# Performance work log

Hardware: AMD Instinct MI355X
Metric: run time of the kernel (lower is better)

The kernel has to match this reference:

```python
import jax, jax.numpy as jnp
import numpy as np

N_NODES = 100000
N_EDGES = 1600000
EMB = 128
EDGE_DIMS = [6, 3]
BN_EPS = 1e-5


def setup_inputs() -> dict:
    key = jax.random.key(0)
    ks = jax.random.split(key, 16)
    inp = {
        "node_feats": jax.random.normal(ks[0], (N_NODES, EMB), jnp.float32),
        "edge_feat_0": jax.random.uniform(ks[1], (N_EDGES, EDGE_DIMS[0]), jnp.float32),
        "edge_feat_1": jax.random.uniform(ks[2], (N_EDGES, EDGE_DIMS[1]), jnp.float32),
        "src": jax.random.randint(ks[3], (N_EDGES,), 0, N_NODES, jnp.int32),
        "dst": jax.random.randint(ks[4], (N_EDGES,), 0, N_NODES, jnp.int32),
    }
    # edge embedding linears (MLP num_layers==1 -> plain Linear)
    s0 = 1.0 / np.sqrt(EDGE_DIMS[0])
    s1 = 1.0 / np.sqrt(EDGE_DIMS[1])
    inp["We0"] = jax.random.uniform(ks[5], (EDGE_DIMS[0], EMB), jnp.float32, -s0, s0)
    inp["be0"] = jax.random.uniform(ks[6], (EMB,), jnp.float32, -s0, s0)
    inp["We1"] = jax.random.uniform(ks[7], (EDGE_DIMS[1], EMB), jnp.float32, -s1, s1)
    inp["be1"] = jax.random.uniform(ks[8], (EMB,), jnp.float32, -s1, s1)
    # mlp: Linear(emb, 2*emb) -> ReLU -> Linear(2*emb, emb)
    sm = 1.0 / np.sqrt(EMB)
    sh = 1.0 / np.sqrt(2 * EMB)
    inp["W1"] = jax.random.uniform(ks[9], (EMB, 2 * EMB), jnp.float32, -sm, sm)
    inp["b1"] = jax.random.uniform(ks[10], (2 * EMB,), jnp.float32, -sm, sm)
    inp["W2"] = jax.random.uniform(ks[11], (2 * EMB, EMB), jnp.float32, -sh, sh)
    inp["b2"] = jax.random.uniform(ks[12], (EMB,), jnp.float32, -sh, sh)
    # batch norm affine params
    inp["gamma"] = jnp.ones((EMB,), jnp.float32)
    inp["beta"] = jnp.zeros((EMB,), jnp.float32)
    return inp


def reference(node_feats, edge_feat_0, edge_feat_1, src, dst,
              We0, be0, We1, be1, W1, b1, W2, b2, gamma, beta):
    n_nodes = node_feats.shape[0]
    # per-family edge embeddings, summed
    edge_embs = (edge_feat_0 @ We0 + be0) + (edge_feat_1 @ We1 + be1)  # [E, D]
    # u_add_e: gather src node feats, add edge emb
    msgs = node_feats[src] + edge_embs  # [E, D]
    # scatter-sum to destination nodes
    agg = jax.ops.segment_sum(msgs, dst, num_segments=n_nodes)  # [N, D]
    # MLP: Linear -> ReLU -> Linear
    h = jax.nn.relu(agg @ W1 + b1) @ W2 + b2  # [N, D]
    # BatchNorm1d (training mode: batch statistics, biased variance)
    mean = jnp.mean(h, axis=0)
    var = jnp.var(h, axis=0)
    h = (h - mean) * jax.lax.rsqrt(var + BN_EPS) * gamma + beta
    return h
```

## Files before the change

kernel.cpp:

```cpp
#include <hip/hip_runtime.h>

#define N_NODES 100000
#define N_EDGES 1600000
#define EMB 128
#define BM 16
#define NSLAB 64
#define BN_EPS 1e-5f

#define SCAN_BLK 512
#define NB_SCAN ((N_NODES + SCAN_BLK - 1) / SCAN_BLK)
#define NPAD (NB_SCAN * SCAN_BLK)

typedef short short8 __attribute__((ext_vector_type(8)));
typedef float floatx4 __attribute__((ext_vector_type(4)));

__device__ __forceinline__ ushort f2bf(float x) {
    unsigned u = __float_as_uint(x);
    u += 0x7fffu + ((u >> 16) & 1u);
    return (ushort)(u >> 16);
}
__device__ __forceinline__ float bf2f(ushort u) {
    return __uint_as_float(((unsigned)u) << 16);
}
__device__ __forceinline__ float lo2f(unsigned p) {
    return __uint_as_float(p << 16);
}
__device__ __forceinline__ float hi2f(unsigned p) {
    return __uint_as_float(p & 0xffff0000u);
}

__global__ __launch_bounds__(256) void setup_kernel(
    const float* __restrict__ nf, ushort* __restrict__ nfbf,
    const int* __restrict__ dst, int* __restrict__ counts,
    const float* __restrict__ W1, const float* __restrict__ W2,
    ushort* __restrict__ w1f, ushort* __restrict__ w2f)
{
    int gtid = blockIdx.x * 256 + threadIdx.x;
    long gstride = (long)gridDim.x * 256;

    if (gtid < 65536) {
        int idx = gtid;
        int i = idx & 7;
        int lane = (idx >> 3) & 63;
        int kloc = ((lane >> 4) << 3) + i;
        int nloc = lane & 15;
        if (idx < 32768) {
            int ks = (idx >> 9) & 3, nt = idx >> 11;
            w1f[idx] = f2bf(W1[(ks * 32 + kloc) * 256 + nt * 16 + nloc]);
        } else {
            int j = idx - 32768;
            int ks = (j >> 9) & 7, nt = j >> 12;
            w2f[j] = f2bf(W2[(ks * 32 + kloc) * 128 + nt * 16 + nloc]);
        }
    }

    long total = (long)N_NODES * EMB / 4;
    for (long p = gtid; p < total; p += gstride) {
        float4 v = ((const float4*)nf)[p];
        ushort4 o;
        o.x = f2bf(v.x); o.y = f2bf(v.y); o.z = f2bf(v.z); o.w = f2bf(v.w);
        ((ushort4*)nfbf)[p] = o;
    }

    for (long e = gtid; e < N_EDGES; e += gstride)
        atomicAdd(&counts[dst[e]], 1);
}

__global__ __launch_bounds__(SCAN_BLK) void scan_blocksum_kernel(
    const int* __restrict__ counts, int* __restrict__ blockSums)
{
    __shared__ int red[SCAN_BLK];
    int t = threadIdx.x;
    int i = blockIdx.x * SCAN_BLK + t;
    red[t] = (i < N_NODES) ? counts[i] : 0;
    __syncthreads();
    for (int s = SCAN_BLK / 2; s > 0; s >>= 1) {
        if (t < s) red[t] += red[t + s];
        __syncthreads();
    }
    if (t == 0) blockSums[blockIdx.x] = red[0];
}

__global__ __launch_bounds__(256) void scan_blockoffsets_kernel(int* __restrict__ blockSums)
{
    __shared__ int s[256];
    int t = threadIdx.x;
    int orig = (t < NB_SCAN) ? blockSums[t] : 0;
    s[t] = orig;
    __syncthreads();
    for (int off = 1; off < 256; off <<= 1) {
        int v = (t >= off) ? s[t - off] : 0;
        __syncthreads();
        s[t] += v;
        __syncthreads();
    }
    if (t < NB_SCAN) blockSums[t] = s[t] - orig;
}

__global__ __launch_bounds__(SCAN_BLK) void scan_final_kernel(
    const int* __restrict__ counts, const int* __restrict__ blockSums,
    int* __restrict__ offsets, int* __restrict__ cursor)
{
    __shared__ int s[SCAN_BLK];
    int t = threadIdx.x;
    int i = blockIdx.x * SCAN_BLK + t;
    int orig = (i < N_NODES) ? counts[i] : 0;
    s[t] = orig;
    __syncthreads();
    for (int off = 1; off < SCAN_BLK; off <<= 1) {
        int v = (t >= off) ? s[t - off] : 0;
        __syncthreads();
        s[t] += v;
        __syncthreads();
    }
    int excl = s[t] - orig + blockSums[blockIdx.x];
    if (i < N_NODES) { offsets[i] = excl; cursor[i] = excl; }
    if (i == N_NODES) offsets[N_NODES] = N_EDGES;
}

__global__ __launch_bounds__(256) void scatter24_kernel(
    const int* __restrict__ src, const int* __restrict__ dst,
    const float* __restrict__ ef0, const float* __restrict__ ef1,
    int* __restrict__ cursor, int* __restrict__ rec24)
{
    int e = blockIdx.x * 256 + threadIdx.x;
    if (e >= N_EDGES) return;
    int t = dst[e];
    int pos = atomicAdd(&cursor[t], 1);

    const float2* p0 = (const float2*)(ef0 + (long)e * 6);
    float2 q0 = p0[0], q1 = p0[1], q2 = p0[2];
    const float* p1 = ef1 + (long)e * 3;
    float g0 = p1[0], g1 = p1[1], g2 = p1[2];

    unsigned u0 = (unsigned)f2bf(q0.x) | ((unsigned)f2bf(q0.y) << 16);
    unsigned u1 = (unsigned)f2bf(q1.x) | ((unsigned)f2bf(q1.y) << 16);
    unsigned u2 = (unsigned)f2bf(q2.x) | ((unsigned)f2bf(q2.y) << 16);
    unsigned u3 = (unsigned)f2bf(g0)   | ((unsigned)f2bf(g1) << 16);
    unsigned u4 = (unsigned)f2bf(g2);

    int2* out = (int2*)(rec24 + (long)pos * 6);
    out[0] = make_int2(src[e], (int)u0);
    out[1] = make_int2((int)u1, (int)u2);
    out[2] = make_int2((int)u3, (int)u4);
}

__global__ __launch_bounds__(256, 8) void gather4_kernel(
    const ushort* __restrict__ nfbf, const int* __restrict__ rec24,
    const int* __restrict__ offsets,
    const float* __restrict__ We0, const float* __restrict__ be0,
    const float* __restrict__ We1, const float* __restrict__ be1,
    float* __restrict__ agg)
{
    int wv = threadIdx.x >> 6, lane = threadIdx.x & 63;
    int n = blockIdx.x * 4 + wv;
    if (n >= N_NODES) return;
    int q = lane >> 4, lp = lane & 15;

    int beg = offsets[n], end = offsets[n + 1];
    float4 accA = make_float4(0.f, 0.f, 0.f, 0.f);
    float4 accB = make_float4(0.f, 0.f, 0.f, 0.f);
    float fs0 = 0.f, fs1 = 0.f, fs2 = 0.f, fs3 = 0.f, fs4 = 0.f,
          fs5 = 0.f, fs6 = 0.f, fs7 = 0.f, fs8 = 0.f;
    const int4* nf16 = (const int4*)nfbf;

    int base = beg;
    for (; base + 64 <= end; base += 64) {
        const int2* rp = (const int2*)(rec24 + (long)(base + lane) * 6);
        int2 ra = rp[0], rb = rp[1], rc = rp[2];
        int sid = ra.x;
        fs0 += lo2f((unsigned)ra.y); fs1 += hi2f((unsigned)ra.y);
        fs2 += lo2f((unsigned)rb.x); fs3 += hi2f((unsigned)rb.x);
        fs4 += lo2f((unsigned)rb.y); fs5 += hi2f((unsigned)rb.y);
        fs6 += lo2f((unsigned)rc.x); fs7 += hi2f((unsigned)rc.x);
        fs8 += lo2f((unsigned)rc.y);
#pragma unroll 4
        for (int j = 0; j < 16; ++j) {
            int s = __shfl(sid, 4 * j + q);
            int4 nv = nf16[(long)s * 16 + lp];
            accA.x += lo2f((unsigned)nv.x); accA.y += hi2f((unsigned)nv.x);
            accA.z += lo2f((unsigned)nv.y); accA.w += hi2f((unsigned)nv.y);
            accB.x += lo2f((unsigned)nv.z); accB.y += hi2f((unsigned)nv.z);
            accB.z += lo2f((unsigned)nv.w); accB.w += hi2f((unsigned)nv.w);
        }
    }
    if (base < end) {
        int m = end - base;
        int sid = 0;
        if (lane < m) {
            const int2* rp = (const int2*)(rec24 + (long)(base + lane) * 6);
            int2 ra = rp[0], rb = rp[1], rc = rp[2];
            sid = ra.x;
            fs0 += lo2f((unsigned)ra.y); fs1 += hi2f((unsigned)ra.y);
            fs2 += lo2f((unsigned)rb.x); fs3 += hi2f((unsigned)rb.x);
            fs4 += lo2f((unsigned)rb.y); fs5 += hi2f((unsigned)rb.y);
            fs6 += lo2f((unsigned)rc.x); fs7 += hi2f((unsigned)rc.x);
            fs8 += lo2f((unsigned)rc.y);
        }
#pragma unroll
        for (int j = 0; j < 16; ++j) {
            int r = 4 * j + q;
            int s = __shfl(sid, r);
            if (r < m) {
                int4 nv = nf16[(long)s * 16 + lp];
                accA.x += lo2f((unsigned)nv.x); accA.y += hi2f((unsigned)nv.x);
                accA.z += lo2f((unsigned)nv.y); accA.w += hi2f((unsigned)nv.y);
                accB.x += lo2f((unsigned)nv.z); accB.y += hi2f((unsigned)nv.z);
                accB.z += lo2f((unsigned)nv.w); accB.w += hi2f((unsigned)nv.w);
            }
        }
    }

    accA.x += __shfl_xor(accA.x, 16); accA.x += __shfl_xor(accA.x, 32);
    accA.y += __shfl_xor(accA.y, 16); accA.y += __shfl_xor(accA.y, 32);
    accA.z += __shfl_xor(accA.z, 16); accA.z += __shfl_xor(accA.z, 32);
    accA.w += __shfl_xor(accA.w, 16); accA.w += __shfl_xor(accA.w, 32);
    accB.x += __shfl_xor(accB.x, 16); accB.x += __shfl_xor(accB.x, 32);
    accB.y += __shfl_xor(accB.y, 16); accB.y += __shfl_xor(accB.y, 32);
    accB.z += __shfl_xor(accB.z, 16); accB.z += __shfl_xor(accB.z, 32);
    accB.w += __shfl_xor(accB.w, 16); accB.w += __shfl_xor(accB.w, 32);

#define WRED(v) v += __shfl_xor(v, 1); v += __shfl_xor(v, 2); v += __shfl_xor(v, 4); \
                v += __shfl_xor(v, 8); v += __shfl_xor(v, 16); v += __shfl_xor(v, 32);
    WRED(fs0) WRED(fs1) WRED(fs2) WRED(fs3) WRED(fs4)
    WRED(fs5) WRED(fs6) WRED(fs7) WRED(fs8)
#undef WRED

    if (q == 0) {
        float deg = (float)(end - beg);
        float4 bA = ((const float4*)be0)[2 * lp];
        float4 bB = ((const float4*)be0)[2 * lp + 1];
        float4 cA = ((const float4*)be1)[2 * lp];
        float4 cB = ((const float4*)be1)[2 * lp + 1];
        float4 eA, eB;
        eA.x = deg * (bA.x + cA.x); eA.y = deg * (bA.y + cA.y);
        eA.z = deg * (bA.z + cA.z); eA.w = deg * (bA.w + cA.w);
        eB.x = deg * (bB.x + cB.x); eB.y = deg * (bB.y + cB.y);
        eB.z = deg * (bB.z + cB.z); eB.w = deg * (bB.w + cB.w);
        float fk[9] = {fs0, fs1, fs2, fs3, fs4, fs5, fs6, fs7, fs8};
#pragma unroll
        for (int k = 0; k < 6; ++k) {
            float4 wA = ((const float4*)We0)[k * 32 + 2 * lp];
            float4 wB = ((const float4*)We0)[k * 32 + 2 * lp + 1];
            eA.x = fmaf(fk[k], wA.x, eA.x); eA.y = fmaf(fk[k], wA.y, eA.y);
            eA.z = fmaf(fk[k], wA.z, eA.z); eA.w = fmaf(fk[k], wA.w, eA.w);
            eB.x = fmaf(fk[k], wB.x, eB.x); eB.y = fmaf(fk[k], wB.y, eB.y);
            eB.z = fmaf(fk[k], wB.z, eB.z); eB.w = fmaf(fk[k], wB.w, eB.w);
        }
#pragma unroll
        for (int k = 0; k < 3; ++k) {
            float4 wA = ((const float4*)We1)[k * 32 + 2 * lp];
            float4 wB = ((const float4*)We1)[k * 32 + 2 * lp + 1];
            eA.x = fmaf(fk[6 + k], wA.x, eA.x); eA.y = fmaf(fk[6 + k], wA.y, eA.y);
            eA.z = fmaf(fk[6 + k], wA.z, eA.z); eA.w = fmaf(fk[6 + k], wA.w, eA.w);
            eB.x = fmaf(fk[6 + k], wB.x, eB.x); eB.y = fmaf(fk[6 + k], wB.y, eB.y);
            eB.z = fmaf(fk[6 + k], wB.z, eB.z); eB.w = fmaf(fk[6 + k], wB.w, eB.w);
        }
        float4 oA = make_float4(accA.x + eA.x, accA.y + eA.y, accA.z + eA.z, accA.w + eA.w);
        float4 oB = make_float4(accB.x + eB.x, accB.y + eB.y, accB.z + eB.z, accB.w + eB.w);
        ((float4*)agg)[(long)n * 32 + 2 * lp] = oA;
        ((float4*)agg)[(long)n * 32 + 2 * lp + 1] = oB;
    }
}

__global__ __launch_bounds__(256) void edge_scatter_kernel(
    const float* __restrict__ node_feats,
    const float* __restrict__ ef0,
    const float* __restrict__ ef1,
    const int* __restrict__ src,
    const int* __restrict__ dst,
    const float* __restrict__ We0, const float* __restrict__ be0,
    const float* __restrict__ We1, const float* __restrict__ be1,
    float* __restrict__ agg)
{
    __shared__ float wS[10 * EMB];
    int tid = threadIdx.x;
    for (int i = tid; i < 6 * EMB; i += 256) wS[i] = We0[i];
    for (int i = tid; i < 3 * EMB; i += 256) wS[6 * EMB + i] = We1[i];
    if (tid < EMB) wS[9 * EMB + tid] = be0[tid] + be1[tid];
    __syncthreads();

    int e = blockIdx.x * 2 + (tid >> 7);
    if (e >= N_EDGES) return;
    int d = tid & 127;
    int s = src[e];
    int t = dst[e];
    const float* f0 = ef0 + (long)e * 6;
    const float* f1 = ef1 + (long)e * 3;

    float emb = wS[9 * EMB + d];
#pragma unroll
    for (int k = 0; k < 6; ++k) emb = fmaf(f0[k], wS[k * EMB + d], emb);
#pragma unroll
    for (int k = 0; k < 3; ++k) emb = fmaf(f1[k], wS[6 * EMB + k * EMB + d], emb);

    float val = node_feats[(long)s * EMB + d] + emb;
    atomicAdd(&agg[(long)t * EMB + d], val);
}

__global__ __launch_bounds__(256) void mlp_mfma_kernel(
    float* __restrict__ h,
    const ushort* __restrict__ w1f, const ushort* __restrict__ w2f,
    const float* __restrict__ b1, const float* __restrict__ b2,
    float* __restrict__ stats)
{
    __shared__ __align__(16) char h1S[32 * 512];

    int tid = threadIdx.x;
    int lane = tid & 63;
    int wv = tid >> 6;
    long base = (long)blockIdx.x * 32;

    float4 araw[2][4][2];
#pragma unroll
    for (int mt = 0; mt < 2; ++mt)
#pragma unroll
        for (int ks = 0; ks < 4; ++ks) {
            long row = base + mt * 16 + (lane & 15);
            const float4* p = (const float4*)(h + row * EMB + ks * 32 + ((lane >> 4) << 3));
            araw[mt][ks][0] = p[0];
            araw[mt][ks][1] = p[1];
        }
    __syncthreads();

    short8 a[2][4];
#pragma unroll
    for (int mt = 0; mt < 2; ++mt)
#pragma unroll
        for (int ks = 0; ks < 4; ++ks) {
            union { ushort u[8]; short8 v; } pk;
            float4 x = araw[mt][ks][0], y = araw[mt][ks][1];
            pk.u[0] = f2bf(x.x); pk.u[1] = f2bf(x.y); pk.u[2] = f2bf(x.z); pk.u[3] = f2bf(x.w);
            pk.u[4] = f2bf(y.x); pk.u[5] = f2bf(y.y); pk.u[6] = f2bf(y.z); pk.u[7] = f2bf(y.w);
            a[mt][ks] = pk.v;
        }

    floatx4 acc1[2][4];
#pragma unroll
    for (int nt = 0; nt < 4; ++nt) {
        float bias = b1[(wv * 4 + nt) * 16 + (lane & 15)];
#pragma unroll
        for (int mt = 0; mt < 2; ++mt)
            acc1[mt][nt] = (floatx4){bias, bias, bias, bias};
    }
#pragma unroll
    for (int ks = 0; ks < 4; ++ks) {
#pragma unroll
        for (int nt = 0; nt < 4; ++nt) {
            short8 b = *(const short8*)&w1f[(((wv * 4 + nt) * 4 + ks) * 64 + lane) * 8];
            acc1[0][nt] = __builtin_amdgcn_mfma_f32_16x16x32_bf16(a[0][ks], b, acc1[0][nt], 0, 0, 0);
            acc1[1][nt] = __builtin_amdgcn_mfma_f32_16x16x32_bf16(a[1][ks], b, acc1[1][nt], 0, 0, 0);
        }
    }
#pragma unroll
    for (int mt = 0; mt < 2; ++mt)
#pragma unroll
        for (int nt = 0; nt < 4; ++nt)
#pragma unroll
            for (int i = 0; i < 4; ++i) {
                int row = mt * 16 + ((lane >> 4) << 2) + i;
                int col = (wv * 4 + nt) * 16 + (lane & 15);
                float v = fmaxf(acc1[mt][nt][i], 0.f);
                *(ushort*)&h1S[row * 512 + ((2 * col) ^ ((row & 7) << 4))] = f2bf(v);
            }
    __syncthreads();

    int swz = (lane & 7) << 4;
    floatx4 acc2[2][2];
#pragma unroll
    for (int nt = 0; nt < 2; ++nt) {
        float bias = b2[(wv * 2 + nt) * 16 + (lane & 15)];
#pragma unroll
        for (int mt = 0; mt < 2; ++mt)
            acc2[mt][nt] = (floatx4){bias, bias, bias, bias};
    }
#pragma unroll
    for (int ks = 0; ks < 8; ++ks) {
        int kb = ks * 64 + ((lane >> 4) << 4);
        short8 a0 = *(const short8*)&h1S[(lane & 15) * 512 + (kb ^ swz)];
        short8 a1 = *(const short8*)&h1S[(16 + (lane & 15)) * 512 + (kb ^ swz)];
#pragma unroll
        for (int nt = 0; nt < 2; ++nt) {
            short8 b = *(const short8*)&w2f[(((wv * 2 + nt) * 8 + ks) * 64 + lane) * 8];
            acc2[0][nt] = __builtin_amdgcn_mfma_f32_16x16x32_bf16(a0, b, acc2[0][nt], 0, 0, 0);
            acc2[1][nt] = __builtin_amdgcn_mfma_f32_16x16x32_bf16(a1, b, acc2[1][nt], 0, 0, 0);
        }
    }

    float s[2] = {0.f, 0.f}, s2[2] = {0.f, 0.f};
#pragma unroll
    for (int nt = 0; nt < 2; ++nt) {
        int col = (wv * 2 + nt) * 16 + (lane & 15);
#pragma unroll
        for (int mt = 0; mt < 2; ++mt)
#pragma unroll
            for (int i = 0; i < 4; ++i) {
                int row = mt * 16 + ((lane >> 4) << 2) + i;
                float v = acc2[mt][nt][i];
                h[(base + row) * EMB + col] = v;
                s[nt] += v;
                s2[nt] = fmaf(v, v, s2[nt]);
            }
    }
#pragma unroll
    for (int nt = 0; nt < 2; ++nt) {
        s[nt] += __shfl_xor(s[nt], 16);
        s[nt] += __shfl_xor(s[nt], 32);
        s2[nt] += __shfl_xor(s2[nt], 16);
        s2[nt] += __shfl_xor(s2[nt], 32);
    }
    if (lane < 16) {
        float* slab = stats + (blockIdx.x & (NSLAB - 1)) * (2 * EMB);
#pragma unroll
        for (int nt = 0; nt < 2; ++nt) {
            int col = (wv * 2 + nt) * 16 + lane;
            atomicAdd(&slab[col], s[nt]);
            atomicAdd(&slab[EMB + col], s2[nt]);
        }
    }
}

__global__ __launch_bounds__(256) void mlp_kernel(
    float* __restrict__ h,
    const float* __restrict__ W1, const float* __restrict__ b1,
    const float* __restrict__ W2, const float* __restrict__ b2,
    float* __restrict__ stats)
{
    __shared__ float aggS[BM][EMB];
    __shared__ float h1S[BM][2 * EMB];
    __shared__ float sredS[256];
    __shared__ float s2redS[256];

    int tid = threadIdx.x;
    long base = (long)blockIdx.x * BM;

    for (int i = tid; i < BM * EMB; i += 256)
        aggS[i >> 7][i & 127] = h[base * EMB + i];
    __syncthreads();

    {
        float acc[BM];
        float bias = b1[tid];
#pragma unroll
        for (int r = 0; r < BM; ++r) acc[r] = bias;
        for (int k = 0; k < EMB; ++k) {
            float w = W1[k * (2 * EMB) + tid];
#pragma unroll
            for (int r = 0; r < BM; ++r) acc[r] = fmaf(aggS[r][k], w, acc[r]);
        }
#pragma unroll
        for (int r = 0; r < BM; ++r) h1S[r][tid] = fmaxf(acc[r], 0.0f);
    }
    __syncthreads();

    {
        int c = tid & 127;
        int half = tid >> 7;
        float acc[8];
        float bias = b2[c];
#pragma unroll
        for (int r = 0; r < 8; ++r) acc[r] = bias;
        for (int k = 0; k < 2 * EMB; ++k) {
            float w = W2[k * EMB + c];
#pragma unroll
            for (int r = 0; r < 8; ++r) acc[r] = fmaf(h1S[half * 8 + r][k], w, acc[r]);
        }
        float s = 0.f, s2 = 0.f;
#pragma unroll
        for (int r = 0; r < 8; ++r) {
            h[(base + half * 8 + r) * EMB + c] = acc[r];
            s += acc[r];
            s2 = fmaf(acc[r], acc[r], s2);
        }
        sredS[tid] = s;
        s2redS[tid] = s2;
    }
    __syncthreads();
    if (tid < 128) {
        float s = sredS[tid] + sredS[tid + 128];
        float s2 = s2redS[tid] + s2redS[tid + 128];
        float* slab = stats + (blockIdx.x & (NSLAB - 1)) * (2 * EMB);
        atomicAdd(&slab[tid], s);
        atomicAdd(&slab[EMB + tid], s2);
    }
}

__global__ __launch_bounds__(256) void bn_apply_fused_kernel(
    float* __restrict__ h, const float* __restrict__ stats,
    const float* __restrict__ gamma, const float* __restrict__ beta)
{
    __shared__ float scS[EMB], shS[EMB];
    int tid = threadIdx.x;
    if (tid < EMB) {
        float s = 0.f, s2 = 0.f;
        for (int b = 0; b < NSLAB; ++b) {
            s += stats[b * (2 * EMB) + tid];
            s2 += stats[b * (2 * EMB) + EMB + tid];
        }
        float mean = s / (float)N_NODES;
        float var = s2 / (float)N_NODES - mean * mean;
        float sc = gamma[tid] * rsqrtf(var + BN_EPS);
        scS[tid] = sc;
        shS[tid] = beta[tid] - mean * sc;
    }
    __syncthreads();
    long total = (long)N_NODES * EMB / 4;
    long stride = (long)gridDim.x * blockDim.x;
    for (long i = (long)blockIdx.x * blockDim.x + threadIdx.x; i < total; i += stride) {
        float4 v = ((float4*)h)[i];
        int c = (int)((i * 4) & 127);
        v.x = fmaf(v.x, scS[c + 0], shS[c + 0]);
        v.y = fmaf(v.y, scS[c + 1], shS[c + 1]);
        v.z = fmaf(v.z, scS[c + 2], shS[c + 2]);
        v.w = fmaf(v.w, scS[c + 3], shS[c + 3]);
        ((float4*)h)[i] = v;
    }
}

extern "C" void kernel_launch(void* const* d_in, const int* in_sizes, int n_in,
                              void* d_out, int out_size, void* d_ws, size_t ws_size,
                              hipStream_t stream) {
    const float* node_feats = (const float*)d_in[0];
    const float* ef0 = (const float*)d_in[1];
    const float* ef1 = (const float*)d_in[2];
    const int* src = (const int*)d_in[3];
    const int* dst = (const int*)d_in[4];
    const float* We0 = (const float*)d_in[5];
    const float* be0 = (const float*)d_in[6];
    const float* We1 = (const float*)d_in[7];
    const float* be1 = (const float*)d_in[8];
    const float* W1 = (const float*)d_in[9];
    const float* b1 = (const float*)d_in[10];
    const float* W2 = (const float*)d_in[11];
    const float* b2 = (const float*)d_in[12];
    const float* gamma = (const float*)d_in[13];
    const float* beta = (const float*)d_in[14];

    float* out = (float*)d_out;

    float* stats = (float*)d_ws;
    float* scaleshift = stats + NSLAB * 2 * EMB;
    int* counts = (int*)(scaleshift + 256);
    int* offsets = counts + NPAD;
    int* cursor = offsets + NPAD;
    int* blockSums = cursor + NPAD;
    ushort* w1f = (ushort*)(blockSums + 256);
    ushort* w2f = w1f + 32768;
    int* rec24 = (int*)(w2f + 32768);
    ushort* nfbf = (ushort*)(rec24 + (size_t)N_EDGES * 6);
    size_t needed = (size_t)((char*)(nfbf + (size_t)N_NODES * EMB) - (char*)d_ws);

    if (ws_size >= needed) {
        hipMemsetAsync(d_ws, 0,
            (size_t)(NSLAB * 2 * EMB + 256) * sizeof(float) + (size_t)NPAD * sizeof(int),
            stream);
        setup_kernel<<<2048, 256, 0, stream>>>(
            node_feats, nfbf, dst, counts, W1, W2, w1f, w2f);
        scan_blocksum_kernel<<<NB_SCAN, SCAN_BLK, 0, stream>>>(counts, blockSums);
        scan_blockoffsets_kernel<<<1, 256, 0, stream>>>(blockSums);
        scan_final_kernel<<<NB_SCAN, SCAN_BLK, 0, stream>>>(counts, blockSums, offsets, cursor);
        scatter24_kernel<<<(N_EDGES + 255) / 256, 256, 0, stream>>>(
            src, dst, ef0, ef1, cursor, rec24);
        gather4_kernel<<<(N_NODES + 3) / 4, 256, 0, stream>>>(
            nfbf, rec24, offsets, We0, be0, We1, be1, out);
        mlp_mfma_kernel<<<N_NODES / 32, 256, 0, stream>>>(
            out, w1f, w2f, b1, b2, stats);
    } else {
        hipMemsetAsync(stats, 0, (size_t)NSLAB * 2 * EMB * sizeof(float), stream);
        hipMemsetAsync(d_out, 0, (size_t)N_NODES * EMB * sizeof(float), stream);
        edge_scatter_kernel<<<N_EDGES / 2, 256, 0, stream>>>(
            node_feats, ef0, ef1, src, dst, We0, be0, We1, be1, out);
        mlp_kernel<<<N_NODES / BM, 256, 0, stream>>>(out, W1, b1, W2, b2, stats);
    }

    bn_apply_fused_kernel<<<4096, 256, 0, stream>>>(out, stats, gamma, beta);
}
```

Baseline: 358.3 us.

## Fuse CSR gather with MFMA MLP and fold block-offset scan into final scan

The per-node gather kernel and the MFMA MLP kernel become one kernel. Each block of 4 waves aggregates 32 nodes, writes the bf16 aggregates into swizzled LDS, then runs both MFMA layers directly from LDS. This removes the fp32 round trip of the aggregate through global memory and one launch. The single-block offset scan is also folded into every final-scan block, which removes another launch at the cost of redundant per-block work. In exchange, each wave now processes 8 nodes serially, the occupancy hint is dropped and LDS use rises, so gather latency hiding may suffer.

```diff
diff --git a/kernel.cpp b/kernel.cpp
--- a/kernel.cpp
+++ b/kernel.cpp
@@ -18,9 +18,6 @@
     unsigned u = __float_as_uint(x);
     u += 0x7fffu + ((u >> 16) & 1u);
     return (ushort)(u >> 16);
-}
-__device__ __forceinline__ float bf2f(ushort u) {
-    return __uint_as_float(((unsigned)u) << 16);
 }
 __device__ __forceinline__ float lo2f(unsigned p) {
     return __uint_as_float(p << 16);
@@ -81,28 +78,23 @@
     if (t == 0) blockSums[blockIdx.x] = red[0];
 }
 
-__global__ __launch_bounds__(256) void scan_blockoffsets_kernel(int* __restrict__ blockSums)
-{
-    __shared__ int s[256];
-    int t = threadIdx.x;
-    int orig = (t < NB_SCAN) ? blockSums[t] : 0;
-    s[t] = orig;
-    __syncthreads();
-    for (int off = 1; off < 256; off <<= 1) {
-        int v = (t >= off) ? s[t - off] : 0;
-        __syncthreads();
-        s[t] += v;
-        __syncthreads();
-    }
-    if (t < NB_SCAN) blockSums[t] = s[t] - orig;
-}
-
 __global__ __launch_bounds__(SCAN_BLK) void scan_final_kernel(
     const int* __restrict__ counts, const int* __restrict__ blockSums,
     int* __restrict__ offsets, int* __restrict__ cursor)
 {
     __shared__ int s[SCAN_BLK];
+    __shared__ int bs[256];
     int t = threadIdx.x;
+    if (t < 256) bs[t] = (t < NB_SCAN) ? blockSums[t] : 0;
+    __syncthreads();
+    for (int off = 1; off < 256; off <<= 1) {
+        int v = (t < 256 && t >= off) ? bs[t - off] : 0;
+        __syncthreads();
+        if (t < 256) bs[t] += v;
+        __syncthreads();
+    }
+    int blockBase = (blockIdx.x == 0) ? 0 : bs[blockIdx.x - 1];
+
     int i = blockIdx.x * SCAN_BLK + t;
     int orig = (i < N_NODES) ? counts[i] : 0;
     s[t] = orig;
@@ -113,7 +105,7 @@
         s[t] += v;
         __syncthreads();
     }
-    int excl = s[t] - orig + blockSums[blockIdx.x];
+    int excl = s[t] - orig + blockBase;
     if (i < N_NODES) { offsets[i] = excl; cursor[i] = excl; }
     if (i == N_NODES) offsets[N_NODES] = N_EDGES;
 }
@@ -145,63 +137,48 @@
     out[2] = make_int2((int)u3, (int)u4);
 }
 
-__global__ __launch_bounds__(256, 8) void gather4_kernel(
+__global__ __launch_bounds__(256) void gather_mlp_kernel(
     const ushort* __restrict__ nfbf, const int* __restrict__ rec24,
     const int* __restrict__ offsets,
     const float* __restrict__ We0, const float* __restrict__ be0,
     const float* __restrict__ We1, const float* __restrict__ be1,
-    float* __restrict__ agg)
-{
-    int wv = threadIdx.x >> 6, lane = threadIdx.x & 63;
-    int n = blockIdx.x * 4 + wv;
-    if (n >= N_NODES) return;
+    const ushort* __restrict__ w1f, const ushort* __restrict__ w2f,
+    const float* __restrict__ b1, const float* __restrict__ b2,
+    float* __restrict__ h, float* __restrict__ stats)
+{
+    __shared__ __align__(16) char aggS[32 * 256];
+    __shared__ __align__(16) char h1S[32 * 512];
+
+    int tid = threadIdx.x;
+    int lane = tid & 63;
+    int wv = tid >> 6;
     int q = lane >> 4, lp = lane & 15;
-
-    int beg = offsets[n], end = offsets[n + 1];
-    float4 accA = make_float4(0.f, 0.f, 0.f, 0.f);
-    float4 accB = make_float4(0.f, 0.f, 0.f, 0.f);
-    float fs0 = 0.f, fs1 = 0.f, fs2 = 0.f, fs3 = 0.f, fs4 = 0.f,
-          fs5 = 0.f, fs6 = 0.f, fs7 = 0.f, fs8 = 0.f;
+    long nbase = (long)blockIdx.x * 32;
     const int4* nf16 = (const int4*)nfbf;
 
-    int base = beg;
-    for (; base + 64 <= end; base += 64) {
-        const int2* rp = (const int2*)(rec24 + (long)(base + lane) * 6);
-        int2 ra = rp[0], rb = rp[1], rc = rp[2];
-        int sid = ra.x;
-        fs0 += lo2f((unsigned)ra.y); fs1 += hi2f((unsigned)ra.y);
-        fs2 += lo2f((unsigned)rb.x); fs3 += hi2f((unsigned)rb.x);
-        fs4 += lo2f((unsigned)rb.y); fs5 += hi2f((unsigned)rb.y);
-        fs6 += lo2f((unsigned)rc.x); fs7 += hi2f((unsigned)rc.x);
-        fs8 += lo2f((unsigned)rc.y);
-#pragma unroll 4
-        for (int j = 0; j < 16; ++j) {
-            int s = __shfl(sid, 4 * j + q);
-            int4 nv = nf16[(long)s * 16 + lp];
-            accA.x += lo2f((unsigned)nv.x); accA.y += hi2f((unsigned)nv.x);
-            accA.z += lo2f((unsigned)nv.y); accA.w += hi2f((unsigned)nv.y);
-            accB.x += lo2f((unsigned)nv.z); accB.y += hi2f((unsigned)nv.z);
-            accB.z += lo2f((unsigned)nv.w); accB.w += hi2f((unsigned)nv.w);
-        }
-    }
-    if (base < end) {
-        int m = end - base;
-        int sid = 0;
-        if (lane < m) {
+#pragma unroll 1
+    for (int t = 0; t < 8; ++t) {
+        int row = wv * 8 + t;
+        int n = (int)nbase + row;
+        int beg = offsets[n], end = offsets[n + 1];
+        float4 accA = make_float4(0.f, 0.f, 0.f, 0.f);
+        float4 accB = make_float4(0.f, 0.f, 0.f, 0.f);
+        float fs0 = 0.f, fs1 = 0.f, fs2 = 0.f, fs3 = 0.f, fs4 = 0.f,
+              fs5 = 0.f, fs6 = 0.f, fs7 = 0.f, fs8 = 0.f;
+
+        int base = beg;
+        for (; base + 64 <= end; base += 64) {
             const int2* rp = (const int2*)(rec24 + (long)(base + lane) * 6);
             int2 ra = rp[0], rb = rp[1], rc = rp[2];
-            sid = ra.x;
+            int sid = ra.x;
             fs0 += lo2f((unsigned)ra.y); fs1 += hi2f((unsigned)ra.y);
             fs2 += lo2f((unsigned)rb.x); fs3 += hi2f((unsigned)rb.x);
             fs4 += lo2f((unsigned)rb.y); fs5 += hi2f((unsigned)rb.y);
             fs6 += lo2f((unsigned)rc.x); fs7 += hi2f((unsigned)rc.x);
             fs8 += lo2f((unsigned)rc.y);
-        }
-#pragma unroll
-        for (int j = 0; j < 16; ++j) {
-            int r = 4 * j + q;
-            int s = __shfl(sid, r);
-            if (r < m) {
+#pragma unroll 4
+            for (int j = 0; j < 16; ++j) {
+                int s = __shfl(sid, 4 * j + q);
                 int4 nv = nf16[(long)s * 16 + lp];
                 accA.x += lo2f((unsigned)nv.x); accA.y += hi2f((unsigned)nv.x);
                 accA.z += lo2f((unsigned)nv.y); accA.w += hi2f((unsigned)nv.y);
@@ -209,57 +186,180 @@
                 accB.z += lo2f((unsigned)nv.w); accB.w += hi2f((unsigned)nv.w);
             }
         }
-    }
-
-    accA.x += __shfl_xor(accA.x, 16); accA.x += __shfl_xor(accA.x, 32);
-    accA.y += __shfl_xor(accA.y, 16); accA.y += __shfl_xor(accA.y, 32);
-    accA.z += __shfl_xor(accA.z, 16); accA.z += __shfl_xor(accA.z, 32);
-    accA.w += __shfl_xor(accA.w, 16); accA.w += __shfl_xor(accA.w, 32);
-    accB.x += __shfl_xor(accB.x, 16); accB.x += __shfl_xor(accB.x, 32);
-    accB.y += __shfl_xor(accB.y, 16); accB.y += __shfl_xor(accB.y, 32);
-    accB.z += __shfl_xor(accB.z, 16); accB.z += __shfl_xor(accB.z, 32);
-    accB.w += __shfl_xor(accB.w, 16); accB.w += __shfl_xor(accB.w, 32);
+        if (base < end) {
+            int m = end - base;
+            int sid = 0;
+            if (lane < m) {
+                const int2* rp = (const int2*)(rec24 + (long)(base + lane) * 6);
+                int2 ra = rp[0], rb = rp[1], rc = rp[2];
+                sid = ra.x;
+                fs0 += lo2f((unsigned)ra.y); fs1 += hi2f((unsigned)ra.y);
+                fs2 += lo2f((unsigned)rb.x); fs3 += hi2f((unsigned)rb.x);
+                fs4 += lo2f((unsigned)rb.y); fs5 += hi2f((unsigned)rb.y);
+                fs6 += lo2f((unsigned)rc.x); fs7 += hi2f((unsigned)rc.x);
+                fs8 += lo2f((unsigned)rc.y);
+            }
+#pragma unroll
+            for (int j = 0; j < 16; ++j) {
+                int r = 4 * j + q;
+                int s = __shfl(sid, r);
+                if (r < m) {
+                    int4 nv = nf16[(long)s * 16 + lp];
+                    accA.x += lo2f((unsigned)nv.x); accA.y += hi2f((unsigned)nv.x);
+                    accA.z += lo2f((unsigned)nv.y); accA.w += hi2f((unsigned)nv.y);
+                    accB.x += lo2f((unsigned)nv.z); accB.y += hi2f((unsigned)nv.z);
+                    accB.z += lo2f((unsigned)nv.w); accB.w += hi2f((unsigned)nv.w);
+                }
+            }
+        }
+
+        accA.x += __shfl_xor(accA.x, 16); accA.x += __shfl_xor(accA.x, 32);
+        accA.y += __shfl_xor(accA.y, 16); accA.y += __shfl_xor(accA.y, 32);
+        accA.z += __shfl_xor(accA.z, 16); accA.z += __shfl_xor(accA.z, 32);
+        accA.w += __shfl_xor(accA.w, 16); accA.w += __shfl_xor(accA.w, 32);
+        accB.x += __shfl_xor(accB.x, 16); accB.x += __shfl_xor(accB.x, 32);
+        accB.y += __shfl_xor(accB.y, 16); accB.y += __shfl_xor(accB.y, 32);
+        accB.z += __shfl_xor(accB.z, 16); accB.z += __shfl_xor(accB.z, 32);
+        accB.w += __shfl_xor(accB.w, 16); accB.w += __shfl_xor(accB.w, 32);
 
 #define WRED(v) v += __shfl_xor(v, 1); v += __shfl_xor(v, 2); v += __shfl_xor(v, 4); \
                 v += __shfl_xor(v, 8); v += __shfl_xor(v, 16); v += __shfl_xor(v, 32);
-    WRED(fs0) WRED(fs1) WRED(fs2) WRED(fs3) WRED(fs4)
-    WRED(fs5) WRED(fs6) WRED(fs7) WRED(fs8)
+        WRED(fs0) WRED(fs1) WRED(fs2) WRED(fs3) WRED(fs4)
+        WRED(fs5) WRED(fs6) WRED(fs7) WRED(fs8)
 #undef WRED
 
-    if (q == 0) {
-        float deg = (float)(end - beg);
-        float4 bA = ((const float4*)be0)[2 * lp];
-        float4 bB = ((const float4*)be0)[2 * lp + 1];
-        float4 cA = ((const float4*)be1)[2 * lp];
-        float4 cB = ((const float4*)be1)[2 * lp + 1];
-        float4 eA, eB;
-        eA.x = deg * (bA.x + cA.x); eA.y = deg * (bA.y + cA.y);
-        eA.z = deg * (bA.z + cA.z); eA.w = deg * (bA.w + cA.w);
-        eB.x = deg * (bB.x + cB.x); eB.y = deg * (bB.y + cB.y);
-        eB.z = deg * (bB.z + cB.z); eB.w = deg * (bB.w + cB.w);
-        float fk[9] = {fs0, fs1, fs2, fs3, fs4, fs5, fs6, fs7, fs8};
-#pragma unroll
-        for (int k = 0; k < 6; ++k) {
-            float4 wA = ((const float4*)We0)[k * 32 + 2 * lp];
-            float4 wB = ((const float4*)We0)[k * 32 + 2 * lp + 1];
-            eA.x = fmaf(fk[k], wA.x, eA.x); eA.y = fmaf(fk[k], wA.y, eA.y);
-            eA.z = fmaf(fk[k], wA.z, eA.z); eA.w = fmaf(fk[k], wA.w, eA.w);
-            eB.x = fmaf(fk[k], wB.x, eB.x); eB.y = fmaf(fk[k], wB.y, eB.y);
-            eB.z = fmaf(fk[k], wB.z, eB.z); eB.w = fmaf(fk[k], wB.w, eB.w);
-        }
-#pragma unroll
-        for (int k = 0; k < 3; ++k) {
-            float4 wA = ((const float4*)We1)[k * 32 + 2 * lp];
-            float4 wB = ((const float4*)We1)[k * 32 + 2 * lp + 1];
-            eA.x = fmaf(fk[6 + k], wA.x, eA.x); eA.y = fmaf(fk[6 + k], wA.y, eA.y);
-            eA.z = fmaf(fk[6 + k], wA.z, eA.z); eA.w = fmaf(fk[6 + k], wA.w, eA.w);
-            eB.x = fmaf(fk[6 + k], wB.x, eB.x); eB.y = fmaf(fk[6 + k], wB.y, eB.y);
-            eB.z = fmaf(fk[6 + k], wB.z, eB.z); eB.w = fmaf(fk[6 + k], wB.w, eB.w);
-        }
-        float4 oA = make_float4(accA.x + eA.x, accA.y + eA.y, accA.z + eA.z, accA.w + eA.w);
-        float4 oB = make_float4(accB.x + eB.x, accB.y + eB.y, accB.z + eB.z, accB.w + eB.w);
-        ((float4*)agg)[(long)n * 32 + 2 * lp] = oA;
-        ((float4*)agg)[(long)n * 32 + 2 * lp + 1] = oB;
+        if (q == 0) {
+            float deg = (float)(end - beg);
+            float4 bA = ((const float4*)be0)[2 * lp];
+            float4 bB = ((const float4*)be0)[2 * lp + 1];
+            float4 cA = ((const float4*)be1)[2 * lp];
+            float4 cB = ((const float4*)be1)[2 * lp + 1];
+            float4 eA, eB;
+            eA.x = deg * (bA.x + cA.x); eA.y = deg * (bA.y + cA.y);
+            eA.z = deg * (bA.z + cA.z); eA.w = deg * (bA.w + cA.w);
+            eB.x = deg * (bB.x + cB.x); eB.y = deg * (bB.y + cB.y);
+            eB.z = deg * (bB.z + cB.z); eB.w = deg * (bB.w + cB.w);
+            float fk[9] = {fs0, fs1, fs2, fs3, fs4, fs5, fs6, fs7, fs8};
+#pragma unroll
+            for (int k = 0; k < 6; ++k) {
+                float4 wA = ((const float4*)We0)[k * 32 + 2 * lp];
+                float4 wB = ((const float4*)We0)[k * 32 + 2 * lp + 1];
+                eA.x = fmaf(fk[k], wA.x, eA.x); eA.y = fmaf(fk[k], wA.y, eA.y);
+                eA.z = fmaf(fk[k], wA.z, eA.z); eA.w = fmaf(fk[k], wA.w, eA.w);
+                eB.x = fmaf(fk[k], wB.x, eB.x); eB.y = fmaf(fk[k], wB.y, eB.y);
+                eB.z = fmaf(fk[k], wB.z, eB.z); eB.w = fmaf(fk[k], wB.w, eB.w);
+            }
+#pragma unroll
+            for (int k = 0; k < 3; ++k) {
+                float4 wA = ((const float4*)We1)[k * 32 + 2 * lp];
+                float4 wB = ((const float4*)We1)[k * 32 + 2 * lp + 1];
+                eA.x = fmaf(fk[6 + k], wA.x, eA.x); eA.y = fmaf(fk[6 + k], wA.y, eA.y);
+                eA.z = fmaf(fk[6 + k], wA.z, eA.z); eA.w = fmaf(fk[6 + k], wA.w, eA.w);
+                eB.x = fmaf(fk[6 + k], wB.x, eB.x); eB.y = fmaf(fk[6 + k], wB.y, eB.y);
+                eB.z = fmaf(fk[6 + k], wB.z, eB.z); eB.w = fmaf(fk[6 + k], wB.w, eB.w);
+            }
+            union { ushort u[8]; short8 v; } pk;
+            pk.u[0] = f2bf(accA.x + eA.x); pk.u[1] = f2bf(accA.y + eA.y);
+            pk.u[2] = f2bf(accA.z + eA.z); pk.u[3] = f2bf(accA.w + eA.w);
+            pk.u[4] = f2bf(accB.x + eB.x); pk.u[5] = f2bf(accB.y + eB.y);
+            pk.u[6] = f2bf(accB.z + eB.z); pk.u[7] = f2bf(accB.w + eB.w);
+            *(short8*)&aggS[row * 256 + ((lp * 16) ^ ((row & 7) << 4))] = pk.v;
+        }
+    }
+    __syncthreads();
+
+    short8 a[2][4];
+#pragma unroll
+    for (int mt = 0; mt < 2; ++mt)
+#pragma unroll
+        for (int ks = 0; ks < 4; ++ks) {
+            int row = (lane & 15) + mt * 16;
+            int kb = ks * 64 + ((lane >> 4) << 4);
+            a[mt][ks] = *(const short8*)&aggS[row * 256 + (kb ^ ((row & 7) << 4))];
+        }
+
+    floatx4 acc1[2][4];
+#pragma unroll
+    for (int nt = 0; nt < 4; ++nt) {
+        float bias = b1[(wv * 4 + nt) * 16 + (lane & 15)];
+#pragma unroll
+        for (int mt = 0; mt < 2; ++mt)
+            acc1[mt][nt] = (floatx4){bias, bias, bias, bias};
+    }
+#pragma unroll
+    for (int ks = 0; ks < 4; ++ks) {
+#pragma unroll
+        for (int nt = 0; nt < 4; ++nt) {
+            short8 b = *(const short8*)&w1f[(((wv * 4 + nt) * 4 + ks) * 64 + lane) * 8];
+            acc1[0][nt] = __builtin_amdgcn_mfma_f32_16x16x32_bf16(a[0][ks], b, acc1[0][nt], 0, 0, 0);
+            acc1[1][nt] = __builtin_amdgcn_mfma_f32_16x16x32_bf16(a[1][ks], b, acc1[1][nt], 0, 0, 0);
+        }
+    }
+#pragma unroll
+    for (int mt = 0; mt < 2; ++mt)
+#pragma unroll
+        for (int nt = 0; nt < 4; ++nt)
+#pragma unroll
+            for (int i = 0; i < 4; ++i) {
+                int row = mt * 16 + ((lane >> 4) << 2) + i;
+                int col = (wv * 4 + nt) * 16 + (lane & 15);
+                float v = fmaxf(acc1[mt][nt][i], 0.f);
+                *(ushort*)&h1S[row * 512 + ((2 * col) ^ ((row & 7) << 4))] = f2bf(v);
+            }
+    __syncthreads();
+
+    int swz = (lane & 7) << 4;
+    floatx4 acc2[2][2];
+#pragma unroll
+    for (int nt = 0; nt < 2; ++nt) {
+        float bias = b2[(wv * 2 + nt) * 16 + (lane & 15)];
+#pragma unroll
+        for (int mt = 0; mt < 2; ++mt)
+            acc2[mt][nt] = (floatx4){bias, bias, bias, bias};
+    }
+#pragma unroll
+    for (int ks = 0; ks < 8; ++ks) {
+        int kb = ks * 64 + ((lane >> 4) << 4);
+        short8 a0 = *(const short8*)&h1S[(lane & 15) * 512 + (kb ^ swz)];
+        short8 a1 = *(const short8*)&h1S[(16 + (lane & 15)) * 512 + (kb ^ swz)];
+#pragma unroll
+        for (int nt = 0; nt < 2; ++nt) {
+            short8 b = *(const short8*)&w2f[(((wv * 2 + nt) * 8 + ks) * 64 + lane) * 8];
+            acc2[0][nt] = __builtin_amdgcn_mfma_f32_16x16x32_bf16(a0, b, acc2[0][nt], 0, 0, 0);
+            acc2[1][nt] = __builtin_amdgcn_mfma_f32_16x16x32_bf16(a1, b, acc2[1][nt], 0, 0, 0);
+        }
+    }
+
+    float s[2] = {0.f, 0.f}, s2[2] = {0.f, 0.f};
+#pragma unroll
+    for (int nt = 0; nt < 2; ++nt) {
+        int col = (wv * 2 + nt) * 16 + (lane & 15);
+#pragma unroll
+        for (int mt = 0; mt < 2; ++mt)
+#pragma unroll
+            for (int i = 0; i < 4; ++i) {
+                int row = mt * 16 + ((lane >> 4) << 2) + i;
+                float v = acc2[mt][nt][i];
+                h[(nbase + row) * EMB + col] = v;
+                s[nt] += v;
+                s2[nt] = fmaf(v, v, s2[nt]);
+            }
+    }
+#pragma unroll
+    for (int nt = 0; nt < 2; ++nt) {
+        s[nt] += __shfl_xor(s[nt], 16);
+        s[nt] += __shfl_xor(s[nt], 32);
+        s2[nt] += __shfl_xor(s2[nt], 16);
+        s2[nt] += __shfl_xor(s2[nt], 32);
+    }
+    if (lane < 16) {
+        float* slab = stats + (blockIdx.x & (NSLAB - 1)) * (2 * EMB);
+#pragma unroll
+        for (int nt = 0; nt < 2; ++nt) {
+            int col = (wv * 2 + nt) * 16 + lane;
+            atomicAdd(&slab[col], s[nt]);
+            atomicAdd(&slab[EMB + col], s2[nt]);
+        }
     }
 }
 
@@ -296,128 +396,6 @@
 
     float val = node_feats[(long)s * EMB + d] + emb;
     atomicAdd(&agg[(long)t * EMB + d], val);
-}
-
-__global__ __launch_bounds__(256) void mlp_mfma_kernel(
-    float* __restrict__ h,
-    const ushort* __restrict__ w1f, const ushort* __restrict__ w2f,
-    const float* __restrict__ b1, const float* __restrict__ b2,
-    float* __restrict__ stats)
-{
-    __shared__ __align__(16) char h1S[32 * 512];
-
-    int tid = threadIdx.x;
-    int lane = tid & 63;
-    int wv = tid >> 6;
-    long base = (long)blockIdx.x * 32;
-
-    float4 araw[2][4][2];
-#pragma unroll
-    for (int mt = 0; mt < 2; ++mt)
-#pragma unroll
-        for (int ks = 0; ks < 4; ++ks) {
-            long row = base + mt * 16 + (lane & 15);
-            const float4* p = (const float4*)(h + row * EMB + ks * 32 + ((lane >> 4) << 3));
-            araw[mt][ks][0] = p[0];
-            araw[mt][ks][1] = p[1];
-        }
-    __syncthreads();
-
-    short8 a[2][4];
-#pragma unroll
-    for (int mt = 0; mt < 2; ++mt)
-#pragma unroll
-        for (int ks = 0; ks < 4; ++ks) {
-            union { ushort u[8]; short8 v; } pk;
-            float4 x = araw[mt][ks][0], y = araw[mt][ks][1];
-            pk.u[0] = f2bf(x.x); pk.u[1] = f2bf(x.y); pk.u[2] = f2bf(x.z); pk.u[3] = f2bf(x.w);
-            pk.u[4] = f2bf(y.x); pk.u[5] = f2bf(y.y); pk.u[6] = f2bf(y.z); pk.u[7] = f2bf(y.w);
-            a[mt][ks] = pk.v;
-        }
-
-    floatx4 acc1[2][4];
-#pragma unroll
-    for (int nt = 0; nt < 4; ++nt) {
-        float bias = b1[(wv * 4 + nt) * 16 + (lane & 15)];
-#pragma unroll
-        for (int mt = 0; mt < 2; ++mt)
-            acc1[mt][nt] = (floatx4){bias, bias, bias, bias};
-    }
-#pragma unroll
-    for (int ks = 0; ks < 4; ++ks) {
-#pragma unroll
-        for (int nt = 0; nt < 4; ++nt) {
-            short8 b = *(const short8*)&w1f[(((wv * 4 + nt) * 4 + ks) * 64 + lane) * 8];
-            acc1[0][nt] = __builtin_amdgcn_mfma_f32_16x16x32_bf16(a[0][ks], b, acc1[0][nt], 0, 0, 0);
-            acc1[1][nt] = __builtin_amdgcn_mfma_f32_16x16x32_bf16(a[1][ks], b, acc1[1][nt], 0, 0, 0);
-        }
-    }
-#pragma unroll
-    for (int mt = 0; mt < 2; ++mt)
-#pragma unroll
-        for (int nt = 0; nt < 4; ++nt)
-#pragma unroll
-            for (int i = 0; i < 4; ++i) {
-                int row = mt * 16 + ((lane >> 4) << 2) + i;
-                int col = (wv * 4 + nt) * 16 + (lane & 15);
-                float v = fmaxf(acc1[mt][nt][i], 0.f);
-                *(ushort*)&h1S[row * 512 + ((2 * col) ^ ((row & 7) << 4))] = f2bf(v);
-            }
-    __syncthreads();
-
-    int swz = (lane & 7) << 4;
-    floatx4 acc2[2][2];
-#pragma unroll
-    for (int nt = 0; nt < 2; ++nt) {
-        float bias = b2[(wv * 2 + nt) * 16 + (lane & 15)];
-#pragma unroll
-        for (int mt = 0; mt < 2; ++mt)
-            acc2[mt][nt] = (floatx4){bias, bias, bias, bias};
-    }
-#pragma unroll
-    for (int ks = 0; ks < 8; ++ks) {
-        int kb = ks * 64 + ((lane >> 4) << 4);
-        short8 a0 = *(const short8*)&h1S[(lane & 15) * 512 + (kb ^ swz)];
-        short8 a1 = *(const short8*)&h1S[(16 + (lane & 15)) * 512 + (kb ^ swz)];
-#pragma unroll
-        for (int nt = 0; nt < 2; ++nt) {
-            short8 b = *(const short8*)&w2f[(((wv * 2 + nt) * 8 + ks) * 64 + lane) * 8];
-            acc2[0][nt] = __builtin_amdgcn_mfma_f32_16x16x32_bf16(a0, b, acc2[0][nt], 0, 0, 0);
-            acc2[1][nt] = __builtin_amdgcn_mfma_f32_16x16x32_bf16(a1, b, acc2[1][nt], 0, 0, 0);
-        }
-    }
-
-    float s[2] = {0.f, 0.f}, s2[2] = {0.f, 0.f};
-#pragma unroll
-    for (int nt = 0; nt < 2; ++nt) {
-        int col = (wv * 2 + nt) * 16 + (lane & 15);
-#pragma unroll
-        for (int mt = 0; mt < 2; ++mt)
-#pragma unroll
-            for (int i = 0; i < 4; ++i) {
-                int row = mt * 16 + ((lane >> 4) << 2) + i;
-                float v = acc2[mt][nt][i];
-                h[(base + row) * EMB + col] = v;
-                s[nt] += v;
-                s2[nt] = fmaf(v, v, s2[nt]);
-            }
-    }
-#pragma unroll
-    for (int nt = 0; nt < 2; ++nt) {
-        s[nt] += __shfl_xor(s[nt], 16);
-        s[nt] += __shfl_xor(s[nt], 32);
-        s2[nt] += __shfl_xor(s2[nt], 16);
-        s2[nt] += __shfl_xor(s2[nt], 32);
-    }
-    if (lane < 16) {
-        float* slab = stats + (blockIdx.x & (NSLAB - 1)) * (2 * EMB);
-#pragma unroll
-        for (int nt = 0; nt < 2; ++nt) {
-            int col = (wv * 2 + nt) * 16 + lane;
-            atomicAdd(&slab[col], s[nt]);
-            atomicAdd(&slab[EMB + col], s2[nt]);
-        }
-    }
 }
 
 __global__ __launch_bounds__(256) void mlp_kernel(
@@ -557,14 +535,11 @@
         setup_kernel<<<2048, 256, 0, stream>>>(
             node_feats, nfbf, dst, counts, W1, W2, w1f, w2f);
         scan_blocksum_kernel<<<NB_SCAN, SCAN_BLK, 0, stream>>>(counts, blockSums);
-        scan_blockoffsets_kernel<<<1, 256, 0, stream>>>(blockSums);
         scan_final_kernel<<<NB_SCAN, SCAN_BLK, 0, stream>>>(counts, blockSums, offsets, cursor);
         scatter24_kernel<<<(N_EDGES + 255) / 256, 256, 0, stream>>>(
             src, dst, ef0, ef1, cursor, rec24);
-        gather4_kernel<<<(N_NODES + 3) / 4, 256, 0, stream>>>(
-            nfbf, rec24, offsets, We0, be0, We1, be1, out);
-        mlp_mfma_kernel<<<N_NODES / 32, 256, 0, stream>>>(
-            out, w1f, w2f, b1, b2, stats);
+        gather_mlp_kernel<<<N_NODES / 32, 256, 0, stream>>>(
+            nfbf, rec24, offsets, We0, be0, We1, be1, w1f, w2f, b1, b2, out, stats);
     } else {
         hipMemsetAsync(stats, 0, (size_t)NSLAB * 2 * EMB * sizeof(float), stream);
         hipMemsetAsync(d_out, 0, (size_t)N_NODES * EMB * sizeof(float), stream);
```

New measurement: 463.7 us. 1.29x slower.
